# Kernel optimization log

Measured on AMD Instinct MI355X. Metric: run time of the kernel, lower is better.

The kernel has to match this reference:

```python
import jax, jax.numpy as jnp
import numpy as np
import math

M = 512          # num_bin_x
NB = 512         # num_bin_y
NUM_NODES = 2_000_000
K = 4            # max bins a node can overlap per dim (size <= 2.5 bins)
SQRT2 = math.sqrt(2.0)


def setup_inputs() -> dict:
    key = jax.random.key(0)
    k1, k2 = jax.random.split(key)
    node_pos = jax.random.uniform(k1, (NUM_NODES, 2), jnp.float32, 0.05, 0.95)
    # node sizes between 0.5 and 2.5 bins (normalized layout units)
    node_size = jax.random.uniform(k2, (NUM_NODES, 2), jnp.float32) * (2.0 / M) + (0.5 / M)
    return {
        "node_pos": node_pos,
        "node_size": node_size,
        "node_weight": jnp.ones((NUM_NODES,), jnp.float32),
        "expand_ratio": jnp.ones((NUM_NODES,), jnp.float32),
        "unit_len": jnp.array([1.0 / M, 1.0 / NB], jnp.float32),
        "init_density_map": jnp.zeros((M, NB), jnp.float32),
        "num_bin_x": M,
        "num_bin_y": NB,
    }


def pre_normalize(node_pos, node_size, node_weight, expand_ratio, unit_len, mx, ny):
    # density_map_cuda.pre_normalize: expand tiny nodes to sqrt(2)*unit_len,
    # rescale weight to preserve area, convert rects to bin coordinates.
    ux, uy = unit_len[0], unit_len[1]
    w, h = node_size[:, 0], node_size[:, 1]
    new_w = jnp.maximum(w, SQRT2 * ux)
    new_h = jnp.maximum(h, SQRT2 * uy)
    weight = node_weight * expand_ratio * (w * h) / (new_w * new_h)
    xl = jnp.clip((node_pos[:, 0] - 0.5 * new_w) / ux, 0.0, mx)
    xh = jnp.clip((node_pos[:, 0] + 0.5 * new_w) / ux, 0.0, mx)
    yl = jnp.clip((node_pos[:, 1] - 0.5 * new_h) / uy, 0.0, ny)
    yh = jnp.clip((node_pos[:, 1] + 0.5 * new_h) / uy, 0.0, ny)
    return jnp.stack([xl, xh, yl, yh, weight], axis=1)  # [N, 5]


def scatter_density(info, mx, ny):
    # density_map_cuda.forward: overlap-area scatter-add of node rects into bins.
    xl, xh, yl, yh, w = info[:, 0], info[:, 1], info[:, 2], info[:, 3], info[:, 4]
    bx0 = jnp.floor(xl).astype(jnp.int32)
    by0 = jnp.floor(yl).astype(jnp.int32)
    dm = jnp.zeros((mx, ny), jnp.float32)
    for dx in range(K):
        ix = bx0 + dx
        fx = ix.astype(jnp.float32)
        ox = jnp.clip(jnp.minimum(xh, fx + 1.0) - jnp.maximum(xl, fx), 0.0)
        ixc = jnp.clip(ix, 0, mx - 1)
        for dy in range(K):
            iy = by0 + dy
            fy = iy.astype(jnp.float32)
            oy = jnp.clip(jnp.minimum(yh, fy + 1.0) - jnp.maximum(yl, fy), 0.0)
            iyc = jnp.clip(iy, 0, ny - 1)
            dm = dm.at[ixc, iyc].add(w * ox * oy)
    return dm


def make_transforms(n):
    k = jnp.arange(n, dtype=jnp.float32)[:, None]
    m = jnp.arange(n, dtype=jnp.float32)[None, :]
    ang = jnp.pi * k * (2.0 * m + 1.0) / (2.0 * n)
    C = jnp.cos(ang)  # [freq, space]
    S = jnp.sin(ang)
    w = jnp.where(jnp.arange(n) == 0, 1.0, 2.0).astype(jnp.float32)
    return C, S, w


def spectral_solve(dm, unit_len, mx, ny):
    # fft_scale construction from __init__
    wj = (jnp.arange(mx, dtype=jnp.float32) * (2.0 * jnp.pi / mx))[:, None]
    wk = (jnp.arange(ny, dtype=jnp.float32) * (2.0 * jnp.pi / ny))[None, :]
    wk = wk * (unit_len[0] / unit_len[1])  # scale_w_k=True
    wsq = wj ** 2 + wk ** 2
    wsq = wsq.at[0, 0].set(1.0)
    pscale = (1.0 / wsq).at[0, 0].set(0.0)
    fx_scale = wj * pscale * 0.5
    fy_scale = wk * pscale * 0.5

    Cx, Sx, wx = make_transforms(mx)
    Cy, Sy, wy = make_transforms(ny)
    # dct2: coeff[u,v] = (1/(M*N)) * sum_{m,n} dm[m,n] cos(pi u(2m+1)/2M) cos(pi v(2n+1)/2N)
    coeff = (Cx @ dm @ Cy.T) / (mx * ny)
    ICx = (wx[:, None] * Cx)  # weighted inverse cosine basis [freq, space]
    ICy = (wy[:, None] * Cy)
    ISx = (wx[:, None] * Sx)
    ISy = (wy[:, None] * Sy)
    potential = ICx.T @ (coeff * pscale) @ ICy          # idct2
    force_x = ISx.T @ (coeff * fx_scale) @ ICy          # idxst_idct
    force_y = ICx.T @ (coeff * fy_scale) @ ISy          # idct_idxst
    return potential, force_x, force_y


def reference(node_pos, node_size, node_weight, expand_ratio, unit_len,
              init_density_map, num_bin_x, num_bin_y):
    info = pre_normalize(node_pos, node_size, node_weight, expand_ratio,
                         unit_len, num_bin_x, num_bin_y)
    density_map = init_density_map + scatter_density(info, num_bin_x, num_bin_y)
    potential, _, _ = spectral_solve(density_map, unit_len, num_bin_x, num_bin_y)
    energy = jnp.sum(potential * density_map)
    return energy
```

## Files before the change

kernel.cpp:

```cpp
#include <hip/hip_runtime.h>
#include <math.h>

#define MX 512
#define NY 512
#define TWO_PI 6.283185307179586f

#define TSHIFT 6
#define NT 64
#define LDIM 68
#define SLAB (LDIM * LDIM)
#define SLAB4 (SLAB / 4)
#define NPB 2048
#define KPT 8
#define CAP 40960
#define SPTMAX 32
#define QSCALE 26214.0f
#define QINV (1.0f / 26214.0f)

typedef __attribute__((ext_vector_type(8))) short short8;
typedef __attribute__((ext_vector_type(4))) float float4_t;
typedef __attribute__((ext_vector_type(4))) unsigned short ushort4_t;

__device__ __forceinline__ unsigned short f2bf(float x) {
    union { float f; unsigned u; } v; v.f = x;
    unsigned r = v.u + 0x7fffu + ((v.u >> 16) & 1u);
    return (unsigned short)(r >> 16);
}
__device__ __forceinline__ float bf2f(unsigned short h) {
    union { float f; unsigned u; } v; v.u = ((unsigned)h) << 16;
    return v.f;
}

__device__ __forceinline__ void node_bounds(float2 p, float2 s, float ux, float uy,
                                            float& xl, float& xh, float& yl, float& yh,
                                            float& nw, float& nh) {
    const float SQ2 = 1.41421356237309515f;
    nw = fmaxf(s.x, SQ2 * ux);
    nh = fmaxf(s.y, SQ2 * uy);
    xl = fminf(fmaxf((p.x - 0.5f * nw) / ux, 0.0f), (float)MX);
    xh = fminf(fmaxf((p.x + 0.5f * nw) / ux, 0.0f), (float)MX);
    yl = fminf(fmaxf((p.y - 0.5f * nh) / uy, 0.0f), (float)NY);
    yh = fminf(fmaxf((p.y + 0.5f * nh) / uy, 0.0f), (float)NY);
}

__global__ void gen_cos_kernel(unsigned short* __restrict__ Ch,
                               unsigned short* __restrict__ Cl,
                               unsigned int* __restrict__ base,
                               unsigned int* __restrict__ cursor,
                               float* __restrict__ out, int cap_mode) {
    int idx = blockIdx.x * blockDim.x + threadIdx.x;
    if (idx == 0) *out = 0.0f;
    if (cap_mode && idx <= NT) {
        base[idx] = (unsigned int)idx * CAP;
        if (idx < NT) cursor[idx] = (unsigned int)idx * CAP;
    }
    int a = idx >> 9;
    int j = idx & 511;
    float x = cospif((float)(a * (2 * j + 1)) * (1.0f / 1024.0f));
    unsigned short hi = f2bf(x);
    Ch[idx] = hi;
    Cl[idx] = f2bf(x - bf2f(hi));
}

__global__ __launch_bounds__(256)
void count_kernel(const float2* __restrict__ pos, const float2* __restrict__ size,
                  const float* __restrict__ unit_len,
                  unsigned int* __restrict__ cnt, int n) {
    __shared__ unsigned int h[NT];
    if (threadIdx.x < NT) h[threadIdx.x] = 0;
    __syncthreads();
    float ux = unit_len[0], uy = unit_len[1];
    int start = blockIdx.x * NPB;
    int end = min(start + NPB, n);
#pragma unroll
    for (int k = 0; k < KPT; k++) {
        int i = start + k * 256 + (int)threadIdx.x;
        if (i < end) {
            float xl, xh, yl, yh, nw, nh;
            node_bounds(pos[i], size[i], ux, uy, xl, xh, yl, yh, nw, nh);
            int bx0 = min((int)floorf(xl), MX - 1);
            int by0 = min((int)floorf(yl), NY - 1);
            atomicAdd(&h[((bx0 >> TSHIFT) << 3) | (by0 >> TSHIFT)], 1u);
        }
    }
    __syncthreads();
    if (threadIdx.x < NT) {
        unsigned int c = h[threadIdx.x];
        if (c) atomicAdd(&cnt[threadIdx.x], c);
    }
}

__global__ void scan_kernel(const unsigned int* __restrict__ cnt,
                            unsigned int* __restrict__ base,
                            unsigned int* __restrict__ cursor) {
    if (threadIdx.x == 0 && blockIdx.x == 0) {
        unsigned int ex = 0;
        for (int t = 0; t < NT; t++) {
            base[t] = ex;
            cursor[t] = ex;
            ex += cnt[t];
        }
        base[NT] = ex;
    }
}

__global__ __launch_bounds__(256)
void place_kernel(const float2* __restrict__ pos, const float2* __restrict__ size,
                  const float* __restrict__ nwt, const float* __restrict__ er,
                  const float* __restrict__ unit_len,
                  const unsigned int* __restrict__ base,
                  unsigned int* __restrict__ cursor,
                  float4* __restrict__ pb, int n) {
    __shared__ unsigned int h[NT];
    __shared__ unsigned int bb[NT];
    if (threadIdx.x < NT) h[threadIdx.x] = 0;
    __syncthreads();
    float ux = unit_len[0], uy = unit_len[1];
    int start = blockIdx.x * NPB;
    int end = min(start + NPB, n);

    float cxl[KPT], cyl[KPT], cw[KPT];
    unsigned int cq[KPT], pk[KPT];
#pragma unroll
    for (int k = 0; k < KPT; k++) {
        int i = start + k * 256 + (int)threadIdx.x;
        if (i < end) {
            float2 p = pos[i], s = size[i];
            float xl, xh, yl, yh, nw, nh;
            node_bounds(p, s, ux, uy, xl, xh, yl, yh, nw, nh);
            cxl[k] = xl; cyl[k] = yl;
            cw[k] = nwt[i] * er[i] * (s.x * s.y) / (nw * nh);
            unsigned qx = (unsigned)((xh - xl) * QSCALE + 0.5f);
            unsigned qy = (unsigned)((yh - yl) * QSCALE + 0.5f);
            if (qx > 65535u) qx = 65535u;
            if (qy > 65535u) qy = 65535u;
            cq[k] = qx | (qy << 16);
            int bx0 = min((int)floorf(xl), MX - 1);
            int by0 = min((int)floorf(yl), NY - 1);
            unsigned int t = ((bx0 >> TSHIFT) << 3) | (by0 >> TSHIFT);
            pk[k] = (t << 11) | atomicAdd(&h[t], 1u);
        }
    }
    __syncthreads();
    if (threadIdx.x < NT) {
        unsigned int c = h[threadIdx.x];
        bb[threadIdx.x] = c ? atomicAdd(&cursor[threadIdx.x], c) : 0u;
    }
    __syncthreads();
#pragma unroll
    for (int k = 0; k < KPT; k++) {
        int i = start + k * 256 + (int)threadIdx.x;
        if (i < end) {
            unsigned int t = pk[k] >> 11;
            unsigned int dst = bb[t] + (pk[k] & 2047u);
            if (dst < base[t + 1])
                pb[dst] = make_float4(cxl[k], cyl[k], cw[k], __uint_as_float(cq[k]));
        }
    }
}

__device__ __forceinline__ void accum_one(float4 v, float* acc, int tbx, int tby) {
    float xl = v.x, yl = v.y, w = v.z;
    unsigned q = __float_as_uint(v.w);
    float xh = xl + (float)(q & 0xffffu) * QINV;
    float yh = yl + (float)(q >> 16) * QINV;
    int bx0 = min((int)floorf(xl), MX - 1);
    int by0 = min((int)floorf(yl), NY - 1);
    float oxs[4], oys[4];
    int rb[4], lys[4];
#pragma unroll
    for (int d = 0; d < 4; d++) {
        int ix = bx0 + d;
        float fx = (float)ix;
        oxs[d] = fmaxf(fminf(xh, fx + 1.0f) - fmaxf(xl, fx), 0.0f);
        rb[d] = (min(ix, MX - 1) - tbx) * LDIM;
        int iy = by0 + d;
        float fy = (float)iy;
        oys[d] = fmaxf(fminf(yh, fy + 1.0f) - fmaxf(yl, fy), 0.0f);
        lys[d] = min(iy, NY - 1) - tby;
    }
#pragma unroll
    for (int dx = 0; dx < 4; dx++) {
        if (oxs[dx] == 0.0f) continue;
        float wox = w * oxs[dx];
#pragma unroll
        for (int dy = 0; dy < 4; dy++) {
            float vv = wox * oys[dy];
            if (vv != 0.0f) atomicAdd(&acc[rb[dx] + lys[dy]], vv);
        }
    }
}

__global__ __launch_bounds__(256)
void accum_kernel(const float4* __restrict__ pb,
                  const unsigned int* __restrict__ base,
                  const unsigned int* __restrict__ cursor,
                  float* __restrict__ slab, int spt) {
    __shared__ float acc[SLAB];
    int t = blockIdx.x / spt;
    int s = blockIdx.x - t * spt;
    int tbx = (t >> 3) << TSHIFT;
    int tby = (t & 7) << TSHIFT;
    for (int e = threadIdx.x; e < SLAB4; e += 256)
        ((float4*)acc)[e] = make_float4(0.f, 0.f, 0.f, 0.f);
    __syncthreads();

    unsigned int b0 = base[t];
    unsigned int c = min(cursor[t] - b0, base[t + 1] - b0);
    unsigned int chunk = (c + spt - 1) / spt;
    unsigned int ks = s * chunk;
    unsigned int ke = min(c, ks + chunk);

    unsigned int k = ks + threadIdx.x;
    float4 cur = make_float4(0.f, 0.f, 0.f, 0.f);
    bool have = (k < ke);
    if (have) cur = pb[b0 + k];
    while (have) {
        unsigned int k2 = k + 256;
        bool have2 = (k2 < ke);
        float4 nxt = make_float4(0.f, 0.f, 0.f, 0.f);
        if (have2) nxt = pb[b0 + k2];
        accum_one(cur, acc, tbx, tby);
        cur = nxt; k = k2; have = have2;
    }
    __syncthreads();

    float4* dst = (float4*)(slab + (size_t)blockIdx.x * SLAB);
    for (int e = threadIdx.x; e < SLAB4; e += 256)
        dst[e] = ((float4*)acc)[e];
}

__global__ __launch_bounds__(256)
void combine_kernel(const float* __restrict__ slab,
                    const float* __restrict__ init_dm,
                    unsigned short* __restrict__ dmh,
                    unsigned short* __restrict__ dml, int spt) {
    int v = blockIdx.x * blockDim.x + threadIdx.x;
    int gx = v >> 7;
    int g4 = v & 127;
    int gy = g4 << 2;
    int rx = gx & 63, ry = gy & 63;
    int tx0 = gx >> TSHIFT, ty0 = gy >> TSHIFT;

    float4 sum = ((const float4*)init_dm)[v];
#pragma unroll
    for (int ax = 0; ax < 2; ax++) {
        int tx = tx0 - ax;
        if (tx < 0 || (ax == 1 && rx > 3)) continue;
        int lx = rx + (ax << TSHIFT);
#pragma unroll
        for (int ay = 0; ay < 2; ay++) {
            int ty = ty0 - ay;
            if (ty < 0 || (ay == 1 && ry > 0)) continue;
            int ly = ry + (ay << TSHIFT);
            const float4* sp = (const float4*)(slab
                + (size_t)(((tx << 3) | ty) * spt) * SLAB + lx * LDIM + ly);
            for (int s = 0; s < spt; s++) {
                float4 sv = sp[(size_t)s * SLAB4];
                sum.x += sv.x; sum.y += sv.y; sum.z += sv.z; sum.w += sv.w;
            }
        }
    }
    ushort4_t hi, lo;
    float sv[4] = {sum.x, sum.y, sum.z, sum.w};
#pragma unroll
    for (int r = 0; r < 4; r++) {
        unsigned short h = f2bf(sv[r]);
        hi[r] = h;
        lo[r] = f2bf(sv[r] - bf2f(h));
    }
    int idx = (gx << 9) | gy;
    *(ushort4_t*)(dmh + idx) = hi;
    *(ushort4_t*)(dml + idx) = lo;
}

__global__ __launch_bounds__(256)
void scatter_kernel(const float2* __restrict__ pos, const float2* __restrict__ size,
                    const float* __restrict__ nwt, const float* __restrict__ er,
                    const float* __restrict__ unit_len,
                    float* __restrict__ dm, int n) {
    int i = blockIdx.x * blockDim.x + threadIdx.x;
    if (i >= n) return;
    float ux = unit_len[0], uy = unit_len[1];
    float2 p = pos[i], s = size[i];
    float xl, xh, yl, yh, nw, nh;
    node_bounds(p, s, ux, uy, xl, xh, yl, yh, nw, nh);
    float w = nwt[i] * er[i] * (s.x * s.y) / (nw * nh);
    int bx0 = (int)floorf(xl);
    int by0 = (int)floorf(yl);
#pragma unroll
    for (int dx = 0; dx < 4; dx++) {
        int ix = bx0 + dx;
        float fx = (float)ix;
        float ox = fmaxf(fminf(xh, fx + 1.0f) - fmaxf(xl, fx), 0.0f);
        if (ox == 0.0f) continue;
        int rowoff = min(max(ix, 0), MX - 1) * NY;
        float wox = w * ox;
#pragma unroll
        for (int dy = 0; dy < 4; dy++) {
            int iy = by0 + dy;
            float fy = (float)iy;
            float oy = fmaxf(fminf(yh, fy + 1.0f) - fmaxf(yl, fy), 0.0f);
            float vv = wox * oy;
            if (vv != 0.0f) atomicAdd(&dm[rowoff + min(max(iy, 0), NY - 1)], vv);
        }
    }
}

__global__ void cvt_dm_kernel(const float* __restrict__ dm,
                              unsigned short* __restrict__ dmh,
                              unsigned short* __restrict__ dml) {
    int idx = blockIdx.x * blockDim.x + threadIdx.x;
    float x = dm[idx];
    unsigned short hi = f2bf(x);
    dmh[idx] = hi;
    dml[idx] = f2bf(x - bf2f(hi));
}

__global__ __launch_bounds__(256)
void dct1_mfma_kernel(const unsigned short* __restrict__ dmh,
                      const unsigned short* __restrict__ dml,
                      const unsigned short* __restrict__ Ch,
                      const unsigned short* __restrict__ Cl,
                      unsigned short* __restrict__ UhT,
                      unsigned short* __restrict__ UlT) {
    int lane = threadIdx.x & 63;
    int wv = threadIdx.x >> 6;
    int tile = blockIdx.x * 4 + wv;
    int jt = (tile >> 5) * 16;
    int bt = (tile & 31) * 16;
    int m = lane & 15, q = lane >> 4;
    float4_t acc = {0.f, 0.f, 0.f, 0.f};
    const unsigned short* ah_row = dmh + (jt + m) * 512;
    const unsigned short* al_row = dml + (jt + m) * 512;
    const unsigned short* bh_row = Ch + (bt + m) * 512;
    const unsigned short* bl_row = Cl + (bt + m) * 512;
#pragma unroll 4
    for (int k0 = 0; k0 < 512; k0 += 32) {
        int off = k0 + q * 8;
        short8 ah = *(const short8*)(ah_row + off);
        short8 al = *(const short8*)(al_row + off);
        short8 bh = *(const short8*)(bh_row + off);
        short8 bl = *(const short8*)(bl_row + off);
        acc = __builtin_amdgcn_mfma_f32_16x16x32_bf16(ah, bh, acc, 0, 0, 0);
        acc = __builtin_amdgcn_mfma_f32_16x16x32_bf16(ah, bl, acc, 0, 0, 0);
        acc = __builtin_amdgcn_mfma_f32_16x16x32_bf16(al, bh, acc, 0, 0, 0);
    }
#pragma unroll
    for (int r = 0; r < 4; r++) {
        float v = acc[r];
        unsigned short hi = f2bf(v);
        int addr = (bt + m) * 512 + jt + q * 4 + r;
        UhT[addr] = hi;
        UlT[addr] = f2bf(v - bf2f(hi));
    }
}

__global__ __launch_bounds__(256)
void dct2_mfma_kernel(const unsigned short* __restrict__ Ch,
                      const unsigned short* __restrict__ Cl,
                      const unsigned short* __restrict__ UhT,
                      const unsigned short* __restrict__ UlT,
                      const float* __restrict__ unit_len,
                      float* __restrict__ out) {
    __shared__ float red[4];
    int lane = threadIdx.x & 63;
    int wv = threadIdx.x >> 6;
    int tile = blockIdx.x * 4 + wv;
    int at = (tile >> 5) * 16;
    int bt = (tile & 31) * 16;
    int m = lane & 15, q = lane >> 4;
    float4_t acc = {0.f, 0.f, 0.f, 0.f};
    const unsigned short* ah_row = Ch + (at + m) * 512;
    const unsigned short* al_row = Cl + (at + m) * 512;
    const unsigned short* bh_row = UhT + (bt + m) * 512;
    const unsigned short* bl_row = UlT + (bt + m) * 512;
#pragma unroll 4
    for (int k0 = 0; k0 < 512; k0 += 32) {
        int off = k0 + q * 8;
        short8 ah = *(const short8*)(ah_row + off);
        short8 al = *(const short8*)(al_row + off);
        short8 bh = *(const short8*)(bh_row + off);
        short8 bl = *(const short8*)(bl_row + off);
        acc = __builtin_amdgcn_mfma_f32_16x16x32_bf16(ah, bh, acc, 0, 0, 0);
        acc = __builtin_amdgcn_mfma_f32_16x16x32_bf16(ah, bl, acc, 0, 0, 0);
        acc = __builtin_amdgcn_mfma_f32_16x16x32_bf16(al, bh, acc, 0, 0, 0);
    }
    float ratio = unit_len[0] / unit_len[1];
    int b = bt + m;
    float wkb = (float)b * (TWO_PI / (float)NY) * ratio;
    float wyb = (b == 0) ? 1.0f : 2.0f;
    float e = 0.0f;
#pragma unroll
    for (int r = 0; r < 4; r++) {
        int a = at + q * 4 + r;
        float wja = (float)a * (TWO_PI / (float)MX);
        float wsq = wja * wja + wkb * wkb;
        float ps = (a == 0 && b == 0) ? 0.0f : (1.0f / wsq);
        float wxa = (a == 0) ? 1.0f : 2.0f;
        e += wxa * wyb * ps * acc[r] * acc[r];
    }
#pragma unroll
    for (int off = 32; off > 0; off >>= 1) e += __shfl_down(e, off, 64);
    if (lane == 0) red[wv] = e;
    __syncthreads();
    if (threadIdx.x == 0) {
        float t = red[0] + red[1] + red[2] + red[3];
        atomicAdd(out, t * (1.0f / ((float)MX * (float)NY)));
    }
}

extern "C" void kernel_launch(void* const* d_in, const int* in_sizes, int n_in,
                              void* d_out, int out_size, void* d_ws, size_t ws_size,
                              hipStream_t stream) {
    const float2* node_pos  = (const float2*)d_in[0];
    const float2* node_size = (const float2*)d_in[1];
    const float*  node_wt   = (const float*)d_in[2];
    const float*  exp_ratio = (const float*)d_in[3];
    const float*  unit_len  = (const float*)d_in[4];
    const float*  init_dm   = (const float*)d_in[5];
    float* out = (float*)d_out;
    int n = in_sizes[2];

    char* wsb = (char*)d_ws;
    size_t off = 0;
    auto alloc = [&](size_t bytes) { void* p = wsb + off; off = (off + bytes + 255) & ~(size_t)255; return p; };
    unsigned short* Ch   = (unsigned short*)alloc((size_t)MX * NY * 2);
    unsigned short* Cl   = (unsigned short*)alloc((size_t)MX * NY * 2);
    unsigned short* dmh  = (unsigned short*)alloc((size_t)MX * NY * 2);
    unsigned short* dml  = (unsigned short*)alloc((size_t)MX * NY * 2);
    unsigned short* UhT  = (unsigned short*)alloc((size_t)MX * NY * 2);
    unsigned short* UlT  = (unsigned short*)alloc((size_t)MX * NY * 2);
    float*          dm     = (float*)alloc((size_t)MX * NY * sizeof(float));
    unsigned int*   cnt    = (unsigned int*)alloc(NT * sizeof(unsigned int));
    unsigned int*   tbase  = (unsigned int*)alloc((NT + 1) * sizeof(unsigned int));
    unsigned int*   cursor = (unsigned int*)alloc(NT * sizeof(unsigned int));
    size_t off_common = off;
    size_t per_spt = (size_t)NT * SLAB * sizeof(float);

    float4* pbF = (float4*)alloc((size_t)NT * CAP * sizeof(float4));
    int sptF = 0;
    float* slbF = nullptr;
    if (off <= ws_size) {
        sptF = (int)((ws_size - off) / per_spt);
        if (sptF > SPTMAX) sptF = SPTMAX;
        if (sptF >= 4) slbF = (float*)alloc((size_t)NT * sptF * SLAB * sizeof(float));
    }
    bool tierFast = (slbF != nullptr);

    off = off_common;
    float4* pbE = (float4*)alloc((size_t)n * sizeof(float4));
    int sptE = 0;
    float* slbE = nullptr;
    if (off <= ws_size) {
        sptE = (int)((ws_size - off) / per_spt);
        if (sptE > SPTMAX) sptE = SPTMAX;
        if (sptE >= 1) slbE = (float*)alloc((size_t)NT * sptE * SLAB * sizeof(float));
    }
    bool tierExact = (slbE != nullptr);

    gen_cos_kernel<<<(MX * NY) / 256, 256, 0, stream>>>(Ch, Cl, tbase, cursor,
                                                        out, tierFast ? 1 : 0);

    if (tierFast || tierExact) {
        float4* pb  = tierFast ? pbF : pbE;
        float*  slb = tierFast ? slbF : slbE;
        int     spt = tierFast ? sptF : sptE;
        int nblk = (n + NPB - 1) / NPB;
        if (!tierFast) {
            hipMemsetAsync(cnt, 0, NT * sizeof(unsigned int), stream);
            count_kernel<<<nblk, 256, 0, stream>>>(node_pos, node_size, unit_len, cnt, n);
            scan_kernel<<<1, 64, 0, stream>>>(cnt, tbase, cursor);
        }
        place_kernel<<<nblk, 256, 0, stream>>>(
            node_pos, node_size, node_wt, exp_ratio, unit_len, tbase, cursor, pb, n);
        accum_kernel<<<NT * spt, 256, 0, stream>>>(pb, tbase, cursor, slb, spt);
        combine_kernel<<<256, 256, 0, stream>>>(slb, init_dm, dmh, dml, spt);
    } else {
        hipMemcpyAsync(dm, init_dm, (size_t)MX * NY * sizeof(float),
                       hipMemcpyDeviceToDevice, stream);
        scatter_kernel<<<(n + 255) / 256, 256, 0, stream>>>(
            node_pos, node_size, node_wt, exp_ratio, unit_len, dm, n);
        cvt_dm_kernel<<<(MX * NY) / 256, 256, 0, stream>>>(dm, dmh, dml);
    }

    dct1_mfma_kernel<<<256, 256, 0, stream>>>(dmh, dml, Ch, Cl, UhT, UlT);
    dct2_mfma_kernel<<<256, 256, 0, stream>>>(Ch, Cl, UhT, UlT, unit_len, out);
}
```

Baseline: 263.7 us.

## Stage binned nodes in LDS for coalesced writes and add parallel slab reduction

```diff
diff --git a/kernel.cpp b/kernel.cpp
--- a/kernel.cpp
+++ b/kernel.cpp
@@ -14,6 +14,7 @@
 #define KPT 8
 #define CAP 40960
 #define SPTMAX 32
+#define RPARTS 19
 #define QSCALE 26214.0f
 #define QINV (1.0f / 26214.0f)
 
@@ -112,7 +113,10 @@
                   unsigned int* __restrict__ cursor,
                   float4* __restrict__ pb, int n) {
     __shared__ unsigned int h[NT];
+    __shared__ unsigned int lb[NT + 1];
     __shared__ unsigned int bb[NT];
+    __shared__ float4 buf[NPB];
+    __shared__ unsigned char til[NPB];
     if (threadIdx.x < NT) h[threadIdx.x] = 0;
     __syncthreads();
     float ux = unit_len[0], uy = unit_len[1];
@@ -142,6 +146,11 @@
         }
     }
     __syncthreads();
+    if (threadIdx.x == 0) {
+        unsigned int ex = 0;
+        for (int t = 0; t < NT; t++) { lb[t] = ex; ex += h[t]; }
+        lb[NT] = ex;
+    }
     if (threadIdx.x < NT) {
         unsigned int c = h[threadIdx.x];
         bb[threadIdx.x] = c ? atomicAdd(&cursor[threadIdx.x], c) : 0u;
@@ -152,10 +161,17 @@
         int i = start + k * 256 + (int)threadIdx.x;
         if (i < end) {
             unsigned int t = pk[k] >> 11;
-            unsigned int dst = bb[t] + (pk[k] & 2047u);
-            if (dst < base[t + 1])
-                pb[dst] = make_float4(cxl[k], cyl[k], cw[k], __uint_as_float(cq[k]));
-        }
+            unsigned int slot = lb[t] + (pk[k] & 2047u);
+            buf[slot] = make_float4(cxl[k], cyl[k], cw[k], __uint_as_float(cq[k]));
+            til[slot] = (unsigned char)t;
+        }
+    }
+    __syncthreads();
+    unsigned int total = lb[NT];
+    for (unsigned int j = threadIdx.x; j < total; j += 256) {
+        unsigned int t = til[j];
+        unsigned int dst = bb[t] + (j - lb[t]);
+        if (dst < base[t + 1]) pb[dst] = buf[j];
     }
 }
 
@@ -231,10 +247,24 @@
 }
 
 __global__ __launch_bounds__(256)
-void combine_kernel(const float* __restrict__ slab,
+void reduce_slabs_kernel(const float* __restrict__ slab,
+                         float* __restrict__ tacc, int spt) {
+    int t = blockIdx.x / RPARTS;
+    int part = blockIdx.x - t * RPARTS;
+    int e = part * 256 + (int)threadIdx.x;
+    if (e < SLAB) {
+        const float* s0 = slab + (size_t)t * spt * SLAB + e;
+        float sum = 0.0f;
+        for (int s = 0; s < spt; s++) sum += s0[(size_t)s * SLAB];
+        tacc[(size_t)t * SLAB + e] = sum;
+    }
+}
+
+__global__ __launch_bounds__(256)
+void combine_kernel(const float* __restrict__ tacc,
                     const float* __restrict__ init_dm,
                     unsigned short* __restrict__ dmh,
-                    unsigned short* __restrict__ dml, int spt) {
+                    unsigned short* __restrict__ dml) {
     int v = blockIdx.x * blockDim.x + threadIdx.x;
     int gx = v >> 7;
     int g4 = v & 127;
@@ -253,12 +283,9 @@
             int ty = ty0 - ay;
             if (ty < 0 || (ay == 1 && ry > 0)) continue;
             int ly = ry + (ay << TSHIFT);
-            const float4* sp = (const float4*)(slab
-                + (size_t)(((tx << 3) | ty) * spt) * SLAB + lx * LDIM + ly);
-            for (int s = 0; s < spt; s++) {
-                float4 sv = sp[(size_t)s * SLAB4];
-                sum.x += sv.x; sum.y += sv.y; sum.z += sv.z; sum.w += sv.w;
-            }
+            float4 sv = *(const float4*)(tacc
+                + (size_t)((tx << 3) | ty) * SLAB + lx * LDIM + ly);
+            sum.x += sv.x; sum.y += sv.y; sum.z += sv.z; sum.w += sv.w;
         }
     }
     ushort4_t hi, lo;
@@ -435,6 +462,7 @@
     unsigned int*   cnt    = (unsigned int*)alloc(NT * sizeof(unsigned int));
     unsigned int*   tbase  = (unsigned int*)alloc((NT + 1) * sizeof(unsigned int));
     unsigned int*   cursor = (unsigned int*)alloc(NT * sizeof(unsigned int));
+    float*          tacc   = (float*)alloc((size_t)NT * SLAB * sizeof(float));
     size_t off_common = off;
     size_t per_spt = (size_t)NT * SLAB * sizeof(float);
 
@@ -475,7 +503,8 @@
         place_kernel<<<nblk, 256, 0, stream>>>(
             node_pos, node_size, node_wt, exp_ratio, unit_len, tbase, cursor, pb, n);
         accum_kernel<<<NT * spt, 256, 0, stream>>>(pb, tbase, cursor, slb, spt);
-        combine_kernel<<<256, 256, 0, stream>>>(slb, init_dm, dmh, dml, spt);
+        reduce_slabs_kernel<<<NT * RPARTS, 256, 0, stream>>>(slb, tacc, spt);
+        combine_kernel<<<256, 256, 0, stream>>>(tacc, init_dm, dmh, dml);
     } else {
         hipMemcpyAsync(dm, init_dm, (size_t)MX * NY * sizeof(float),
                        hipMemcpyDeviceToDevice, stream);
```

Measured after the change: 240.5 us. 1.1x faster.
